# Kernel optimization log

Hardware: AMD Instinct MI355X
Metric: run time of the kernel (lower is better)

The kernel has to match this reference:

```python
import jax, jax.numpy as jnp
import numpy as np

B, T, N, M, D = 4, 64, 16, 8, 512

def setup_inputs() -> dict:
    key = jax.random.key(0)
    ks = jax.random.split(key, 7)
    s = 1.0 / np.sqrt(D)
    return {
        "x": jax.random.normal(ks[0], (B, T, N, M, D), dtype=jnp.float32),
        "Wq": jax.random.normal(ks[1], (D, D), dtype=jnp.float32) * s,
        "bq": jax.random.normal(ks[2], (D,), dtype=jnp.float32) * s,
        "Wk": jax.random.normal(ks[3], (D, D), dtype=jnp.float32) * s,
        "bk": jax.random.normal(ks[4], (D,), dtype=jnp.float32) * s,
        "Wv": jax.random.normal(ks[5], (D, D), dtype=jnp.float32) * s,
        "bv": jax.random.normal(ks[6], (D,), dtype=jnp.float32) * s,
    }

def reference(x, Wq, bq, Wk, bk, Wv, bv):
    # Linear projections (torch Linear: y = x @ W^T + b)
    Q = jnp.einsum('btnmd,ed->btnme', x, Wq) + bq
    K = jnp.einsum('btnmd,ed->btnme', x, Wk) + bk
    V = jnp.einsum('btnmd,ed->btnme', x, Wv) + bv
    scale = 1.0 / jnp.sqrt(jnp.asarray(Q.shape[-1], Q.dtype))
    # contract over batch b AND feature d -> shared attention over modality axis m
    attn_score = jnp.einsum('btnmd,btnkd->tnmk', Q, K) * scale  # [t,n,m,m]
    attn_weight = jax.nn.softmax(attn_score, axis=-1)
    return jnp.einsum('tnmk,btnkd->btnmd', attn_weight, V)
```

## Files before the change

### kernel.cpp

```cpp
#include <hip/hip_runtime.h>

#define Bb 4
#define Tt 64
#define Nn 16
#define Mm 8
#define Dd 512
#define RR 32
#define QSTR 536
#define VOFF 270336

typedef __attribute__((ext_vector_type(8))) short bf16x8;
typedef __attribute__((ext_vector_type(16))) float f32x16;

__device__ __forceinline__ unsigned short f2bf(float f) {
    union { float f; unsigned int u; } v; v.f = f;
    unsigned int r = (v.u + 0x7fffu + ((v.u >> 16) & 1u)) >> 16;
    return (unsigned short)r;
}
__device__ __forceinline__ float bf2f(unsigned short h) {
    union { unsigned int u; float f; } v; v.u = ((unsigned int)h) << 16;
    return v.f;
}

__global__ __launch_bounds__(256) void pack_wv_kernel(
    const float* __restrict__ Wv, unsigned short* __restrict__ Wb)
{
    int idx = blockIdx.x * 256 + threadIdx.x;
    int o = idx << 2;
    int j  = o & 7;
    int n  = (o >> 3) & 31;
    int hi = (o >> 8) & 1;
    int ekk = o >> 9;
    int kk = ekk & 31;
    int e  = ekk >> 5;
    int row = e * 32 + n;
    int d = kk * 16 + hi * 8 + j;
    float4 v = *(const float4*)(Wv + row * Dd + d);
    ushort4 o4;
    o4.x = f2bf(v.x); o4.y = f2bf(v.y); o4.z = f2bf(v.z); o4.w = f2bf(v.w);
    *(ushort4*)(Wb + VOFF + o) = o4;
}

__global__ __launch_bounds__(256) void pack_bqk_kernel(
    const float* __restrict__ Wq, const float* __restrict__ Wk,
    const float* __restrict__ bq, unsigned short* __restrict__ Wb)
{
    __shared__ unsigned short lq[512 * 32];
    __shared__ unsigned short lk[512 * 32];
    const int tid = threadIdx.x;
    const int eT = blockIdx.x & 15;
    const int dT = blockIdx.x >> 4;

    #pragma unroll
    for (int i = 0; i < 16; ++i) {
        int fi = i * 256 + tid;
        int n = fi >> 3;
        int c4 = (fi & 7) << 2;
        float4 vq = *(const float4*)(Wq + n * Dd + dT * 32 + c4);
        float4 vk = *(const float4*)(Wk + n * Dd + eT * 32 + c4);
        ushort4 a, b;
        a.x = f2bf(vq.x); a.y = f2bf(vq.y); a.z = f2bf(vq.z); a.w = f2bf(vq.w);
        b.x = f2bf(vk.x); b.y = f2bf(vk.y); b.z = f2bf(vk.z); b.w = f2bf(vk.w);
        *(ushort4*)(&lq[n * 32 + c4]) = a;
        *(ushort4*)(&lk[n * 32 + c4]) = b;
    }
    __syncthreads();

    {
        int dp = tid & 31;
        int e0 = (tid >> 5) << 2;
        float acc0 = 0.f, acc1 = 0.f, acc2 = 0.f, acc3 = 0.f;
        for (int n = 0; n < 512; ++n) {
            float a = bf2f(lq[n * 32 + dp]);
            acc0 += a * bf2f(lk[n * 32 + e0 + 0]);
            acc1 += a * bf2f(lk[n * 32 + e0 + 1]);
            acc2 += a * bf2f(lk[n * 32 + e0 + 2]);
            acc3 += a * bf2f(lk[n * 32 + e0 + 3]);
        }
        int kk = dT * 2 + (dp >> 4);
        int k16 = dp & 15;
        int h = k16 >> 3, j = k16 & 7;
        long base = ((long)(eT * 33 + kk) << 9) + ((h * 32) << 3) + j;
        Wb[base + ((e0 + 0) << 3)] = f2bf(acc0);
        Wb[base + ((e0 + 1) << 3)] = f2bf(acc1);
        Wb[base + ((e0 + 2) << 3)] = f2bf(acc2);
        Wb[base + ((e0 + 3) << 3)] = f2bf(acc3);
    }

    if (dT == 0) {
        long b32 = (long)(eT * 33 + 32) << 9;
        if (tid < 256) { Wb[b32 + tid] = 0; Wb[b32 + 256 + tid] = 0; }
        __syncthreads();
        if (tid < 32) {
            float c = 0.f;
            for (int n = 0; n < 512; ++n) c += bf2f(lk[n * 32 + tid]) * bq[n];
            Wb[b32 + (tid << 3)] = f2bf(c);
        }
    }
}

__global__ __launch_bounds__(1024, 4) void fused_attn_kernel(
    const float* __restrict__ x, const unsigned short* __restrict__ Wb,
    const float* __restrict__ bv, float* __restrict__ out)
{
    __shared__ unsigned short lds_x[2][RR * QSTR];
    __shared__ float lds_s[2][64];

    const int tid = threadIdx.x;
    const int lane = tid & 63;
    const int wave = tid >> 6;
    const int arow = lane & 31;
    const int ahalf = lane >> 5;
    const int l5 = lane & 31;

    const int gi0 = blockIdx.x << 1;
    const int t = gi0 >> 4;
    const int n0 = gi0 & 15;
    const int rot = (blockIdx.x * 7) & 31;

    const unsigned short* wb = Wb + (long)wave * (33 * 512) + (lane << 3);
    #define KOF(s) ((s) + rot >= 32 ? (s) + rot - 32 : (s) + rot)

    bf16x8 pf[4];
    pf[0] = *(const bf16x8*)(wb + KOF(0) * 512);
    pf[1] = *(const bf16x8*)(wb + KOF(1) * 512);
    pf[2] = *(const bf16x8*)(wb + KOF(2) * 512);
    pf[3] = *(const bf16x8*)(wb + KOF(3) * 512);

    if (tid < 128) lds_s[tid >> 6][tid & 63] = 0.f;

    #pragma unroll
    for (int i = 0; i < 8; ++i) {
        int fi = i * 1024 + tid;
        int g = fi >> 12;
        int rem = fi & 4095;
        int row = rem >> 7;
        int d = (rem & 127) << 2;
        int b = row >> 3, m = row & 7;
        float4 v = *(const float4*)(x + ((((long)(b * Tt + t)) * Nn + (n0 + g)) * Mm + m) * Dd + d);
        ushort4 o;
        o.x = f2bf(v.x); o.y = f2bf(v.y); o.z = f2bf(v.z); o.w = f2bf(v.w);
        *(ushort4*)(&lds_x[g][row * QSTR + d]) = o;
    }
    if (tid < 64) {
        int g = tid >> 5, row = tid & 31;
        unsigned short* p = &lds_x[g][row * QSTR + 512];
        ushort4 one = {0x3F80, 0, 0, 0}, zz = {0, 0, 0, 0};
        *(ushort4*)(p) = one; *(ushort4*)(p + 4) = zz;
        *(ushort4*)(p + 8) = zz; *(ushort4*)(p + 12) = zz;
    }
    __syncthreads();

    const unsigned short* abase0 = &lds_x[0][arow * QSTR + (ahalf << 3)];
    const unsigned short* abase1 = &lds_x[1][arow * QSTR + (ahalf << 3)];

    f32x16 aY0, aY1;
    #pragma unroll
    for (int r = 0; r < 16; ++r) { aY0[r] = 0.f; aY1[r] = 0.f; }

    #pragma unroll
    for (int s = 0; s < 33; ++s) {
        int kk = (s < 32) ? KOF(s) : 32;
        bf16x8 bf = pf[s & 3];
        if (s + 4 <= 32) {
            int kn = (s + 4 < 32) ? KOF(s + 4) : 32;
            pf[s & 3] = *(const bf16x8*)(wb + kn * 512);
        }
        bf16x8 a0 = *(const bf16x8*)(abase0 + kk * 16);
        bf16x8 a1 = *(const bf16x8*)(abase1 + kk * 16);
        aY0 = __builtin_amdgcn_mfma_f32_32x32x16_bf16(a0, bf, aY0, 0, 0, 0);
        aY1 = __builtin_amdgcn_mfma_f32_32x32x16_bf16(a1, bf, aY1, 0, 0, 0);
    }

    const int ecol = (wave << 5) + l5;
    #pragma unroll
    for (int g = 0; g < 2; ++g) {
        const f32x16& aY = g ? aY1 : aY0;
        float p[32];
        #pragma unroll
        for (int i = 0; i < 32; ++i) p[i] = 0.f;
        #pragma unroll
        for (int b = 0; b < 4; ++b) {
            float xc[8];
            #pragma unroll
            for (int k = 0; k < 8; ++k)
                xc[k] = bf2f(lds_x[g][(b * 8 + k) * QSTR + ecol]);
            #pragma unroll
            for (int mm = 0; mm < 4; ++mm) {
                float yv = aY[b * 4 + mm];
                #pragma unroll
                for (int k = 0; k < 8; ++k) p[mm * 8 + k] += yv * xc[k];
            }
        }
        const bool b0 = (lane & 1) != 0;
        const bool b1 = (lane & 2) != 0;
        const bool b2 = (lane & 4) != 0;
        const bool b3 = (lane & 8) != 0;
        const bool b4 = (lane & 16) != 0;
        float q16[16];
        #pragma unroll
        for (int i = 0; i < 16; ++i) {
            float keep = b0 ? p[2 * i + 1] : p[2 * i];
            float send = b0 ? p[2 * i] : p[2 * i + 1];
            q16[i] = keep + __shfl_xor(send, 1);
        }
        float q8[8];
        #pragma unroll
        for (int i = 0; i < 8; ++i) {
            float keep = b1 ? q16[2 * i + 1] : q16[2 * i];
            float send = b1 ? q16[2 * i] : q16[2 * i + 1];
            q8[i] = keep + __shfl_xor(send, 2);
        }
        float q4[4];
        #pragma unroll
        for (int i = 0; i < 4; ++i) {
            float keep = b2 ? q8[2 * i + 1] : q8[2 * i];
            float send = b2 ? q8[2 * i] : q8[2 * i + 1];
            q4[i] = keep + __shfl_xor(send, 4);
        }
        float q2[2];
        #pragma unroll
        for (int i = 0; i < 2; ++i) {
            float keep = b3 ? q4[2 * i + 1] : q4[2 * i];
            float send = b3 ? q4[2 * i] : q4[2 * i + 1];
            q2[i] = keep + __shfl_xor(send, 8);
        }
        float sval = (b4 ? q2[1] : q2[0]) + __shfl_xor(b4 ? q2[0] : q2[1], 16);
        int k = l5 & 7, mm = l5 >> 3;
        int m = mm + 4 * ahalf;
        atomicAdd(&lds_s[g][m * 8 + k], sval);
    }

    const unsigned short* vb = Wb + VOFF + ((long)wave << 14) + (lane << 3);
    bf16x8 pv[4];
    pv[0] = *(const bf16x8*)(vb + ((0 + rot) & 31) * 512);
    pv[1] = *(const bf16x8*)(vb + ((1 + rot) & 31) * 512);
    pv[2] = *(const bf16x8*)(vb + ((2 + rot) & 31) * 512);
    pv[3] = *(const bf16x8*)(vb + ((3 + rot) & 31) * 512);

    __syncthreads();

    if (tid < 128) {
        int g = tid >> 6;
        int p = tid & 63;
        float s = lds_s[g][p] * 0.04419417382415922f;
        float mx = s;
        mx = fmaxf(mx, __shfl_xor(mx, 1));
        mx = fmaxf(mx, __shfl_xor(mx, 2));
        mx = fmaxf(mx, __shfl_xor(mx, 4));
        float e = __expf(s - mx);
        float sum = e;
        sum += __shfl_xor(sum, 1);
        sum += __shfl_xor(sum, 2);
        sum += __shfl_xor(sum, 4);
        lds_s[g][p] = e / sum;
    }
    __syncthreads();

    {
        int d4 = tid & 127;
        int b = (tid >> 7) & 3;
        int g = tid >> 9;
        unsigned short* xr = &lds_x[g][(b << 3) * QSTR + (d4 << 2)];
        float4 xv[8];
        #pragma unroll
        for (int k = 0; k < 8; ++k) {
            ushort4 u = *(const ushort4*)(xr + k * QSTR);
            xv[k].x = bf2f(u.x); xv[k].y = bf2f(u.y);
            xv[k].z = bf2f(u.z); xv[k].w = bf2f(u.w);
        }
        ushort4 yr[8];
        #pragma unroll
        for (int m = 0; m < 8; ++m) {
            float4 o = {0.f, 0.f, 0.f, 0.f};
            #pragma unroll
            for (int k = 0; k < 8; ++k) {
                float w = lds_s[g][(m << 3) + k];
                o.x += w * xv[k].x; o.y += w * xv[k].y;
                o.z += w * xv[k].z; o.w += w * xv[k].w;
            }
            ushort4 oy;
            oy.x = f2bf(o.x); oy.y = f2bf(o.y); oy.z = f2bf(o.z); oy.w = f2bf(o.w);
            yr[m] = oy;
        }
        #pragma unroll
        for (int m = 0; m < 8; ++m) *(ushort4*)(xr + m * QSTR) = yr[m];
    }
    __syncthreads();

    {
        f32x16 aV0, aV1;
        #pragma unroll
        for (int r = 0; r < 16; ++r) { aV0[r] = 0.f; aV1[r] = 0.f; }
        #pragma unroll
        for (int s = 0; s < 32; ++s) {
            int kk = (s + rot) & 31;
            bf16x8 wvf = pv[s & 3];
            if (s + 4 < 32) pv[s & 3] = *(const bf16x8*)(vb + (((s + 4 + rot) & 31)) * 512);
            bf16x8 a0 = *(const bf16x8*)(abase0 + kk * 16);
            bf16x8 a1 = *(const bf16x8*)(abase1 + kk * 16);
            aV0 = __builtin_amdgcn_mfma_f32_32x32x16_bf16(a0, wvf, aV0, 0, 0, 0);
            aV1 = __builtin_amdgcn_mfma_f32_32x32x16_bf16(a1, wvf, aV1, 0, 0, 0);
        }
        int f = (wave << 5) + arow;
        float bvv = bv[f];
        float* o0 = out + f;
        #pragma unroll
        for (int r = 0; r < 16; ++r) {
            int mrow = (r & 3) + 8 * (r >> 2) + 4 * ahalf;
            int b = mrow >> 3, m = mrow & 7;
            long base = ((((long)(b * Tt + t)) * Nn + n0) * Mm + m) * Dd;
            o0[base] = aV0[r] + bvv;
            o0[base + (long)Mm * Dd] = aV1[r] + bvv;
        }
    }
    #undef KOF
}

extern "C" void kernel_launch(void* const* d_in, const int* in_sizes, int n_in,
                              void* d_out, int out_size, void* d_ws, size_t ws_size,
                              hipStream_t stream) {
    const float* x  = (const float*)d_in[0];
    const float* Wq = (const float*)d_in[1];
    const float* bq = (const float*)d_in[2];
    const float* Wk = (const float*)d_in[3];
    const float* bv = (const float*)d_in[6];
    const float* Wv = (const float*)d_in[5];
    float* out = (float*)d_out;
    unsigned short* Wb = (unsigned short*)d_ws;

    pack_wv_kernel<<<256, 256, 0, stream>>>(Wv, Wb);
    pack_bqk_kernel<<<256, 256, 0, stream>>>(Wq, Wk, bq, Wb);
    fused_attn_kernel<<<Tt * Nn / 2, 1024, 0, stream>>>(x, Wb, bv, out);
}
```

Baseline: 201.7 us.

## Merge weight pack kernels and compute Wq^T·Wk product with MFMA

Folds the two weight-preprocessing kernels into one launch, with the Wv packing handled by extra blocks. The Wq^T·Wk product is now computed with bf16 MFMA instructions and a cross-wave LDS reduction instead of a scalar FMA loop over 512 terms. The bias term is computed in parallel strips and reduced. In the fused attention kernel, the weight prefetch depth goes from 4 to 6 fragments, which adds register pressure. The MFMA path loads Wq/Wk as strided scalar global reads rather than through LDS.

```diff
diff --git a/kernel.cpp b/kernel.cpp
--- a/kernel.cpp
+++ b/kernel.cpp
@@ -22,79 +22,86 @@
     return v.f;
 }
 
-__global__ __launch_bounds__(256) void pack_wv_kernel(
-    const float* __restrict__ Wv, unsigned short* __restrict__ Wb)
+__global__ __launch_bounds__(256) void pack_kernel(
+    const float* __restrict__ Wq, const float* __restrict__ Wk,
+    const float* __restrict__ Wv, const float* __restrict__ bq,
+    unsigned short* __restrict__ Wb)
 {
-    int idx = blockIdx.x * 256 + threadIdx.x;
-    int o = idx << 2;
-    int j  = o & 7;
-    int n  = (o >> 3) & 31;
-    int hi = (o >> 8) & 1;
-    int ekk = o >> 9;
-    int kk = ekk & 31;
-    int e  = ekk >> 5;
-    int row = e * 32 + n;
-    int d = kk * 16 + hi * 8 + j;
-    float4 v = *(const float4*)(Wv + row * Dd + d);
-    ushort4 o4;
-    o4.x = f2bf(v.x); o4.y = f2bf(v.y); o4.z = f2bf(v.z); o4.w = f2bf(v.w);
-    *(ushort4*)(Wb + VOFF + o) = o4;
-}
-
-__global__ __launch_bounds__(256) void pack_bqk_kernel(
-    const float* __restrict__ Wq, const float* __restrict__ Wk,
-    const float* __restrict__ bq, unsigned short* __restrict__ Wb)
-{
-    __shared__ unsigned short lq[512 * 32];
-    __shared__ unsigned short lk[512 * 32];
     const int tid = threadIdx.x;
+    if (blockIdx.x >= 256) {
+        int idx = (blockIdx.x - 256) * 256 + tid;
+        int o = idx << 2;
+        int j  = o & 7;
+        int n  = (o >> 3) & 31;
+        int hi = (o >> 8) & 1;
+        int ekk = o >> 9;
+        int kk = ekk & 31;
+        int e  = ekk >> 5;
+        int row = e * 32 + n;
+        int d = kk * 16 + hi * 8 + j;
+        float4 v = *(const float4*)(Wv + row * Dd + d);
+        ushort4 o4;
+        o4.x = f2bf(v.x); o4.y = f2bf(v.y); o4.z = f2bf(v.z); o4.w = f2bf(v.w);
+        *(ushort4*)(Wb + VOFF + o) = o4;
+        return;
+    }
+
     const int eT = blockIdx.x & 15;
     const int dT = blockIdx.x >> 4;
-
-    #pragma unroll
-    for (int i = 0; i < 16; ++i) {
-        int fi = i * 256 + tid;
-        int n = fi >> 3;
-        int c4 = (fi & 7) << 2;
-        float4 vq = *(const float4*)(Wq + n * Dd + dT * 32 + c4);
-        float4 vk = *(const float4*)(Wk + n * Dd + eT * 32 + c4);
-        ushort4 a, b;
-        a.x = f2bf(vq.x); a.y = f2bf(vq.y); a.z = f2bf(vq.z); a.w = f2bf(vq.w);
-        b.x = f2bf(vk.x); b.y = f2bf(vk.y); b.z = f2bf(vk.z); b.w = f2bf(vk.w);
-        *(ushort4*)(&lq[n * 32 + c4]) = a;
-        *(ushort4*)(&lk[n * 32 + c4]) = b;
-    }
-    __syncthreads();
-
-    {
-        int dp = tid & 31;
-        int e0 = (tid >> 5) << 2;
-        float acc0 = 0.f, acc1 = 0.f, acc2 = 0.f, acc3 = 0.f;
-        for (int n = 0; n < 512; ++n) {
-            float a = bf2f(lq[n * 32 + dp]);
-            acc0 += a * bf2f(lk[n * 32 + e0 + 0]);
-            acc1 += a * bf2f(lk[n * 32 + e0 + 1]);
-            acc2 += a * bf2f(lk[n * 32 + e0 + 2]);
-            acc3 += a * bf2f(lk[n * 32 + e0 + 3]);
-        }
-        int kk = dT * 2 + (dp >> 4);
-        int k16 = dp & 15;
-        int h = k16 >> 3, j = k16 & 7;
-        long base = ((long)(eT * 33 + kk) << 9) + ((h * 32) << 3) + j;
-        Wb[base + ((e0 + 0) << 3)] = f2bf(acc0);
-        Wb[base + ((e0 + 1) << 3)] = f2bf(acc1);
-        Wb[base + ((e0 + 2) << 3)] = f2bf(acc2);
-        Wb[base + ((e0 + 3) << 3)] = f2bf(acc3);
+    const int wave = tid >> 6, lane = tid & 63;
+    const int arow = lane & 31, h = lane >> 5;
+
+    f32x16 acc;
+    #pragma unroll
+    for (int r = 0; r < 16; ++r) acc[r] = 0.f;
+
+    #pragma unroll
+    for (int s = 0; s < 8; ++s) {
+        int n0 = (wave * 8 + s) * 16;
+        bf16x8 af, bfr;
+        #pragma unroll
+        for (int j = 0; j < 8; ++j) {
+            int n = n0 + h * 8 + j;
+            af[j]  = (short)f2bf(Wq[n * Dd + dT * 32 + arow]);
+            bfr[j] = (short)f2bf(Wk[n * Dd + eT * 32 + arow]);
+        }
+        acc = __builtin_amdgcn_mfma_f32_32x32x16_bf16(af, bfr, acc, 0, 0, 0);
+    }
+
+    __shared__ float red[4][1024];
+    #pragma unroll
+    for (int r = 0; r < 16; ++r) {
+        int row = (r & 3) + 8 * (r >> 2) + 4 * h;
+        red[wave][row * 32 + arow] = acc[r];
+    }
+    __syncthreads();
+
+    #pragma unroll
+    for (int i = 0; i < 4; ++i) {
+        int el = i * 256 + tid;
+        int dp = el >> 5, ep = el & 31;
+        float v = red[0][el] + red[1][el] + red[2][el] + red[3][el];
+        int d = dT * 32 + dp;
+        int kkg = d >> 4, hh = (d >> 3) & 1, jj = d & 7;
+        Wb[(long)(eT * 33 + kkg) * 512 + ((hh * 32 + ep) << 3) + jj] = f2bf(v);
     }
 
     if (dT == 0) {
+        int ep = tid & 31, strip = tid >> 5;
+        float c = 0.f;
+        #pragma unroll 8
+        for (int n = strip * 64; n < strip * 64 + 64; ++n)
+            c += bf2f(f2bf(Wk[n * Dd + eT * 32 + ep])) * bq[n];
+        __syncthreads();
+        red[0][tid] = c;
         long b32 = (long)(eT * 33 + 32) << 9;
-        if (tid < 256) { Wb[b32 + tid] = 0; Wb[b32 + 256 + tid] = 0; }
+        Wb[b32 + tid] = 0; Wb[b32 + 256 + tid] = 0;
         __syncthreads();
         if (tid < 32) {
-            float c = 0.f;
-            for (int n = 0; n < 512; ++n) c += bf2f(lk[n * 32 + tid]) * bq[n];
-            Wb[b32 + (tid << 3)] = f2bf(c);
+            float s = 0.f;
+            #pragma unroll
+            for (int k = 0; k < 8; ++k) s += red[0][k * 32 + tid];
+            Wb[b32 + (tid << 3)] = f2bf(s);
         }
     }
 }
@@ -121,11 +128,10 @@
     const unsigned short* wb = Wb + (long)wave * (33 * 512) + (lane << 3);
     #define KOF(s) ((s) + rot >= 32 ? (s) + rot - 32 : (s) + rot)
 
-    bf16x8 pf[4];
-    pf[0] = *(const bf16x8*)(wb + KOF(0) * 512);
-    pf[1] = *(const bf16x8*)(wb + KOF(1) * 512);
-    pf[2] = *(const bf16x8*)(wb + KOF(2) * 512);
-    pf[3] = *(const bf16x8*)(wb + KOF(3) * 512);
+    bf16x8 pf[6];
+    #pragma unroll
+    for (int i = 0; i < 6; ++i)
+        pf[i] = *(const bf16x8*)(wb + KOF(i) * 512);
 
     if (tid < 128) lds_s[tid >> 6][tid & 63] = 0.f;
 
@@ -161,10 +167,10 @@
     #pragma unroll
     for (int s = 0; s < 33; ++s) {
         int kk = (s < 32) ? KOF(s) : 32;
-        bf16x8 bf = pf[s & 3];
-        if (s + 4 <= 32) {
-            int kn = (s + 4 < 32) ? KOF(s + 4) : 32;
-            pf[s & 3] = *(const bf16x8*)(wb + kn * 512);
+        bf16x8 bf = pf[s % 6];
+        if (s + 6 <= 32) {
+            int kn = (s + 6 < 32) ? KOF(s + 6) : 32;
+            pf[s % 6] = *(const bf16x8*)(wb + kn * 512);
         }
         bf16x8 a0 = *(const bf16x8*)(abase0 + kk * 16);
         bf16x8 a1 = *(const bf16x8*)(abase1 + kk * 16);
@@ -324,12 +330,11 @@
     const float* Wq = (const float*)d_in[1];
     const float* bq = (const float*)d_in[2];
     const float* Wk = (const float*)d_in[3];
+    const float* Wv = (const float*)d_in[5];
     const float* bv = (const float*)d_in[6];
-    const float* Wv = (const float*)d_in[5];
     float* out = (float*)d_out;
     unsigned short* Wb = (unsigned short*)d_ws;
 
-    pack_wv_kernel<<<256, 256, 0, stream>>>(Wv, Wb);
-    pack_bqk_kernel<<<256, 256, 0, stream>>>(Wq, Wk, bq, Wb);
+    pack_kernel<<<512, 256, 0, stream>>>(Wq, Wk, Wv, bq, Wb);
     fused_attn_kernel<<<Tt * Nn / 2, 1024, 0, stream>>>(x, Wb, bv, out);
 }
```

After: 169.4 us. 1.19x faster.
